# Performance work log

Measured on AMD Instinct MI355X. Metric: run time of the kernel, lower is better.

## Reference

```python
import jax, jax.numpy as jnp
import numpy as np

CHAN = 128
IN_CHAN = 3
NB_OUT = 10
K = 2  # maxPoolKer


def affine_grid(theta, H, W):
    # theta: [C,2,3] -> grid [C,H,W,2], torch F.affine_grid align_corners=False
    xs = (2.0 * jnp.arange(W, dtype=jnp.float32) + 1.0) / W - 1.0
    ys = (2.0 * jnp.arange(H, dtype=jnp.float32) + 1.0) / H - 1.0
    gx, gy = jnp.meshgrid(xs, ys)  # [H,W]
    base = jnp.stack([gx, gy, jnp.ones_like(gx)], axis=-1)  # [H,W,3]
    return jnp.einsum('crk,hwk->chwr', theta, base)  # [...,0]=x, [...,1]=y


def grid_sample(img, grid):
    # img [M,H,W], grid [M,H,W,2]; bilinear, zeros padding, align_corners=False
    M, H, W = img.shape
    ix = ((grid[..., 0] + 1.0) * W - 1.0) * 0.5
    iy = ((grid[..., 1] + 1.0) * H - 1.0) * 0.5
    x0 = jnp.floor(ix)
    y0 = jnp.floor(iy)
    wx = ix - x0
    wy = iy - y0

    def tap(xi, yi):
        valid = (xi >= 0) & (xi <= W - 1) & (yi >= 0) & (yi <= H - 1)
        xc = jnp.clip(xi, 0, W - 1).astype(jnp.int32)
        yc = jnp.clip(yi, 0, H - 1).astype(jnp.int32)
        v = jax.vmap(lambda im, y, x: im[y, x])(img, yc, xc)
        return jnp.where(valid, v, 0.0)

    v00 = tap(x0, y0)
    v01 = tap(x0 + 1.0, y0)
    v10 = tap(x0, y0 + 1.0)
    v11 = tap(x0 + 1.0, y0 + 1.0)
    return (1.0 - wy) * ((1.0 - wx) * v00 + wx * v01) + wy * ((1.0 - wx) * v10 + wx * v11)


def geom_layer(x, geo, lin, box):
    # x [B,Ci,H,W]; lin [C,Ci]; geo,box [C,2,3]
    B, Ci, H, W = x.shape
    C = lin.shape[0]
    y = jnp.einsum('ci,bihw->bchw', lin, x)  # channel linear combine
    grid = affine_grid(geo, H, W)            # [C,H,W,2], shared across batch
    samp = jax.vmap(lambda yb: grid_sample(yb, grid))(y)  # [B,C,H,W]
    bgrid = affine_grid(box, H, W)
    boxm = grid_sample(jnp.ones((C, H, W), samp.dtype), bgrid)  # BoxPool mask
    return samp * boxm[None]


def maxpool_g(x, k):
    # MaxPool2d_G: depthwise box-filter conv -> argmax -> gather window from padded x
    B, C, H, W = x.shape
    ch, cw = H // k, W // k
    ker = jnp.ones((1, 1, ch, cw), x.dtype) / (ch + cw)
    xr = x.reshape(B * C, 1, H, W)
    conv = jax.lax.conv_general_dilated(
        xr, ker, (1, 1), [(ch // 2, ch // 2), (cw // 2, cw // 2)])
    conv = conv[:, :, :H, :W].reshape(B, C, H * W)
    argm = jnp.argmax(conv, axis=-1)
    r = argm // H  # original code uses origImgSize[0]; assumes square H==W
    c = argm % W
    padH, padW = H + H // k, W + W // k
    top = padH // 2 - H // 2
    left = padW // 2 - W // 2
    padded = jnp.zeros((B, C, padH, padW), x.dtype).at[:, :, top:top + H, left:left + W].set(x)
    r2 = r + H // (2 * k)
    c2 = c + W // (2 * k)
    ri = r2[..., None] + (jnp.arange(ch) - ch // 2)  # [B,C,ch]
    ci = c2[..., None] + (jnp.arange(cw) - cw // 2)  # [B,C,cw]
    gat = jax.vmap(jax.vmap(lambda p, rr, cc: p[rr[:, None], cc[None, :]]))(padded, ri, ci)
    return gat  # [B,C,ch,cw]


def setup_inputs() -> dict:
    key = jax.random.key(0)
    ks = jax.random.split(key, 12)
    eye = jnp.eye(3, dtype=jnp.float32)[:2]  # [2,3]
    x = jax.random.normal(ks[0], (8, IN_CHAN, 64, 64), dtype=jnp.float32)
    geo0 = eye[None] + 0.1 * jax.random.normal(ks[1], (CHAN, 2, 3), dtype=jnp.float32)
    lin0 = jax.random.uniform(ks[2], (CHAN, IN_CHAN), dtype=jnp.float32)
    box0 = eye[None] + 0.1 * jax.random.normal(ks[3], (CHAN, 2, 3), dtype=jnp.float32)
    geos = eye[None, None] + 0.1 * jax.random.normal(ks[4], (3, CHAN, 2, 3), dtype=jnp.float32)
    lins = jax.random.uniform(ks[5], (3, CHAN, CHAN), dtype=jnp.float32)
    boxes = eye[None, None] + 0.1 * jax.random.normal(ks[6], (3, CHAN, 2, 3), dtype=jnp.float32)
    bound = 1.0 / np.sqrt(CHAN)
    dense_w = jax.random.uniform(ks[7], (NB_OUT, CHAN), dtype=jnp.float32, minval=-bound, maxval=bound)
    dense_b = jax.random.uniform(ks[8], (NB_OUT,), dtype=jnp.float32, minval=-bound, maxval=bound)
    return {"x": x, "geo0": geo0, "lin0": lin0, "box0": box0,
            "geos": geos, "lins": lins, "boxes": boxes,
            "dense_w": dense_w, "dense_b": dense_b}


def reference(x, geo0, lin0, box0, geos, lins, boxes, dense_w, dense_b):
    h = geom_layer(x, geo0, lin0, box0)            # inLay: [8,128,64,64]
    h = geom_layer(h, geos[0], lins[0], boxes[0])  # layer 0
    h = maxpool_g(h, K)                            # layer 1 (maxPoolPos=1): [8,128,32,32]
    h = geom_layer(h, geos[1], lins[1], boxes[1])  # layer 2
    h = geom_layer(h, geos[2], lins[2], boxes[2])  # layer 3
    feat = h
    pooled = feat.mean(axis=-1).mean(axis=-1)      # [B,C]
    out = pooled @ dense_w.T + dense_b             # [B,nbOut]
    return out, feat
```

## Files before the change

### kernel.cpp

```cpp
#include <hip/hip_runtime.h>

#define BB 8
#define CC 128

__device__ __forceinline__ float sample_pad(const float* __restrict__ pl, int stride,
                                            float WF, float ix, float iy) {
  ix = fminf(fmaxf(ix, -1.0f), WF);
  iy = fminf(fmaxf(iy, -1.0f), WF);
  float x0f = floorf(ix), y0f = floorf(iy);
  float wx = ix - x0f, wy = iy - y0f;
  int xi = (int)x0f + 1, yi = (int)y0f + 1;
  const float* p0 = pl + yi * stride + xi;
  float v00 = p0[0], v01 = p0[1], v10 = p0[stride], v11 = p0[stride + 1];
  return (1.0f - wy) * ((1.0f - wx) * v00 + wx * v01) +
         wy * ((1.0f - wx) * v10 + wx * v11);
}

__device__ __forceinline__ float box_mask(float bix, float biy, float WM1) {
  float bx0 = floorf(bix), by0 = floorf(biy);
  float bwx = bix - bx0, bwy = biy - by0;
  float mx = (((bx0 >= 0.0f) && (bx0 <= WM1)) ? (1.0f - bwx) : 0.0f) +
             (((bx0 >= -1.0f) && (bx0 <= WM1 - 1.0f)) ? bwx : 0.0f);
  float my = (((by0 >= 0.0f) && (by0 <= WM1)) ? (1.0f - bwy) : 0.0f) +
             (((by0 >= -1.0f) && (by0 <= WM1 - 1.0f)) ? bwy : 0.0f);
  return mx * my;
}

__global__ __launch_bounds__(256) void inlay_sample_kernel(
    const float* __restrict__ x, const float* __restrict__ lin,
    const float* __restrict__ geo, const float* __restrict__ box,
    const float* __restrict__ db, float* __restrict__ out,
    float* __restrict__ head) {
  const int H = 64, W = 64, HW = 4096;
  __shared__ float cp[67 * 68];
  int bc = blockIdx.x;
  int c = bc & (CC - 1);
  int b = bc >> 7;
  int tid = threadIdx.x;
  if (bc == 0 && tid < 80) head[tid] = db[tid % 10];
  const float* xb = x + (size_t)b * 3 * HW;

  float w0 = lin[c * 3 + 0], w1 = lin[c * 3 + 1], w2 = lin[c * 3 + 2];

  if (tid < 68) {
    cp[tid] = 0.0f; cp[65 * 68 + tid] = 0.0f; cp[66 * 68 + tid] = 0.0f;
  } else if (tid < 132) {
    int r = tid - 67;
    cp[r * 68 + 0] = 0.0f; cp[r * 68 + 65] = 0.0f; cp[r * 68 + 66] = 0.0f;
  }

#pragma unroll
  for (int k = 0; k < 4; ++k) {
    int i4 = tid + k * 256;
    int base = i4 * 4;
    float4 f0 = *reinterpret_cast<const float4*>(&xb[base]);
    float4 f1 = *reinterpret_cast<const float4*>(&xb[HW + base]);
    float4 f2 = *reinterpret_cast<const float4*>(&xb[2 * HW + base]);
    int h = i4 >> 4, w = (i4 & 15) * 4;
    float* d = &cp[(h + 1) * 68 + w + 1];
    d[0] = w0 * f0.x + w1 * f1.x + w2 * f2.x;
    d[1] = w0 * f0.y + w1 * f1.y + w2 * f2.y;
    d[2] = w0 * f0.z + w1 * f1.z + w2 * f2.z;
    d[3] = w0 * f0.w + w1 * f1.w + w2 * f2.w;
  }
  __syncthreads();

  const float* g = geo + c * 6;
  const float* bx = box + c * 6;
  float g0 = g[0], g1 = g[1], g2 = g[2], g3 = g[3], g4 = g[4], g5 = g[5];
  float b0 = bx[0], b1 = bx[1], b2 = bx[2], b3 = bx[3], b4 = bx[4], b5 = bx[5];
  float* o = out + ((size_t)b * CC + c) * HW;

#pragma unroll
  for (int k = 0; k < 16; ++k) {
    int px = tid + k * 256;
    int h = px >> 6, w = px & 63;
    float xs = (2.0f * w + 1.0f) / W - 1.0f;
    float ys = (2.0f * h + 1.0f) / H - 1.0f;
    float ix = ((g0 * xs + g1 * ys + g2 + 1.0f) * W - 1.0f) * 0.5f;
    float iy = ((g3 * xs + g4 * ys + g5 + 1.0f) * H - 1.0f) * 0.5f;
    float samp = sample_pad(cp, 68, 64.0f, ix, iy);
    float bix = ((b0 * xs + b1 * ys + b2 + 1.0f) * W - 1.0f) * 0.5f;
    float biy = ((b3 * xs + b4 * ys + b5 + 1.0f) * H - 1.0f) * 0.5f;
    o[px] = samp * box_mask(bix, biy, 63.0f);
  }
}

__global__ __launch_bounds__(256) void gemm64_kernel(
    const float* __restrict__ lin, const float* __restrict__ x,
    float* __restrict__ y, int HW) {
  const int Ci = 128;
  __shared__ __align__(16) float As[16][68];
  __shared__ __align__(16) float Bs[16][64];
  int b = blockIdx.z;
  const float* xb = x + (size_t)b * Ci * HW;
  float* yb = y + (size_t)b * CC * HW;
  int tid = threadIdx.x;
  int tx = tid & 15, ty = tid >> 4;
  int row0 = blockIdx.y * 64;
  int col0 = blockIdx.x * 64;
  int m = tid >> 2, kq = (tid & 3) * 4;
  int kk = tid >> 4, n4 = (tid & 15) * 4;
  float acc[4][4] = {};
  float4 ra = *reinterpret_cast<const float4*>(&lin[(row0 + m) * Ci + kq]);
  float4 rb = *reinterpret_cast<const float4*>(&xb[(size_t)kk * HW + col0 + n4]);
  for (int k0 = 0; k0 < 128; k0 += 16) {
    __syncthreads();
    As[kq + 0][m] = ra.x; As[kq + 1][m] = ra.y; As[kq + 2][m] = ra.z; As[kq + 3][m] = ra.w;
    *reinterpret_cast<float4*>(&Bs[kk][n4]) = rb;
    __syncthreads();
    if (k0 + 16 < 128) {
      ra = *reinterpret_cast<const float4*>(&lin[(row0 + m) * Ci + k0 + 16 + kq]);
      rb = *reinterpret_cast<const float4*>(&xb[(size_t)(k0 + 16 + kk) * HW + col0 + n4]);
    }
#pragma unroll
    for (int kki = 0; kki < 16; ++kki) {
      float4 a4 = *reinterpret_cast<const float4*>(&As[kki][ty * 4]);
      float4 b4 = *reinterpret_cast<const float4*>(&Bs[kki][tx * 4]);
      float a[4] = {a4.x, a4.y, a4.z, a4.w};
      float bv[4] = {b4.x, b4.y, b4.z, b4.w};
#pragma unroll
      for (int i = 0; i < 4; i++)
#pragma unroll
        for (int j = 0; j < 4; j++) acc[i][j] += a[i] * bv[j];
    }
  }
#pragma unroll
  for (int i = 0; i < 4; i++) {
    float* yr = yb + (size_t)(row0 + ty * 4 + i) * HW + col0 + tx * 4;
    *reinterpret_cast<float4*>(yr) = make_float4(acc[i][0], acc[i][1], acc[i][2], acc[i][3]);
  }
}

__global__ __launch_bounds__(256) void sampmax_kernel(
    const float* __restrict__ y, const float* __restrict__ geo,
    const float* __restrict__ box, float* __restrict__ out) {
  __shared__ __align__(16) float sp[64 * 68];
  __shared__ __align__(16) float arena[67 * 68];
  __shared__ float wv[4];
  __shared__ int wi[4];
  __shared__ int am_s;
  float* pl = arena;
  float* cb = arena;

  int bc = blockIdx.x;
  int c = bc & (CC - 1);
  int tid = threadIdx.x;

  if (tid < 68) {
    pl[tid] = 0.0f; pl[65 * 68 + tid] = 0.0f; pl[66 * 68 + tid] = 0.0f;
  } else if (tid < 132) {
    int r = tid - 67;
    pl[r * 68 + 0] = 0.0f; pl[r * 68 + 65] = 0.0f; pl[r * 68 + 66] = 0.0f;
  }
  {
    const float* plane = y + (size_t)bc * 4096;
#pragma unroll
    for (int k = 0; k < 4; ++k) {
      int i4 = tid + k * 256;
      float4 f = *reinterpret_cast<const float4*>(&plane[i4 * 4]);
      int h = i4 >> 4, w = (i4 & 15) * 4;
      float* d = &pl[(h + 1) * 68 + w + 1];
      d[0] = f.x; d[1] = f.y; d[2] = f.z; d[3] = f.w;
    }
  }
  __syncthreads();

  {
    const float* g = geo + c * 6;
    const float* bx = box + c * 6;
    float g0 = g[0], g1 = g[1], g2 = g[2], g3 = g[3], g4 = g[4], g5 = g[5];
    float b0 = bx[0], b1 = bx[1], b2 = bx[2], b3 = bx[3], b4 = bx[4], b5 = bx[5];
#pragma unroll
    for (int k = 0; k < 16; ++k) {
      int px = tid + k * 256;
      int h = px >> 6, w = px & 63;
      float xs = (2.0f * w + 1.0f) / 64.0f - 1.0f;
      float ys = (2.0f * h + 1.0f) / 64.0f - 1.0f;
      float ix = ((g0 * xs + g1 * ys + g2 + 1.0f) * 64.0f - 1.0f) * 0.5f;
      float iy = ((g3 * xs + g4 * ys + g5 + 1.0f) * 64.0f - 1.0f) * 0.5f;
      float samp = sample_pad(pl, 68, 64.0f, ix, iy);
      float bix = ((b0 * xs + b1 * ys + b2 + 1.0f) * 64.0f - 1.0f) * 0.5f;
      float biy = ((b3 * xs + b4 * ys + b5 + 1.0f) * 64.0f - 1.0f) * 0.5f;
      sp[h * 68 + w] = samp * box_mask(bix, biy, 63.0f);
    }
  }
  __syncthreads();

  {
    int strip = tid >> 4, w4 = (tid & 15) * 4;
    int h0 = strip * 4;
    float4 a = make_float4(0.f, 0.f, 0.f, 0.f);
    float4 keep0 = a, keep1 = a, keep2 = a;
#pragma unroll
    for (int j = 0; j < 32; ++j) {
      int r = h0 + j - 16;
      bool valid = (r >= 0) && (r < 64);
      int rc = valid ? r : 0;
      float4 f = *reinterpret_cast<const float4*>(&sp[rc * 68 + w4]);
      f.x = valid ? f.x : 0.0f; f.y = valid ? f.y : 0.0f;
      f.z = valid ? f.z : 0.0f; f.w = valid ? f.w : 0.0f;
      if (j == 0) keep0 = f;
      if (j == 1) keep1 = f;
      if (j == 2) keep2 = f;
      a.x += f.x; a.y += f.y; a.z += f.z; a.w += f.w;
    }
    *reinterpret_cast<float4*>(&cb[(h0 + 0) * 68 + w4]) = a;
#pragma unroll
    for (int j = 32; j < 35; ++j) {
      int r = h0 + j - 16;
      bool valid = (r < 64);
      int rc = valid ? r : 0;
      float4 f = *reinterpret_cast<const float4*>(&sp[rc * 68 + w4]);
      f.x = valid ? f.x : 0.0f; f.y = valid ? f.y : 0.0f;
      f.z = valid ? f.z : 0.0f; f.w = valid ? f.w : 0.0f;
      float4 kp = (j == 32) ? keep0 : ((j == 33) ? keep1 : keep2);
      a.x += f.x - kp.x; a.y += f.y - kp.y; a.z += f.z - kp.z; a.w += f.w - kp.w;
      *reinterpret_cast<float4*>(&cb[(h0 + j - 31) * 68 + w4]) = a;
    }
  }
  __syncthreads();

  float best = -3.402823466e+38f;
  int bidx = 0x7fffffff;
#pragma unroll
  for (int hh = 0; hh < 4; ++hh) {
    int h = (tid >> 4) + hh * 16;
    int w4 = (tid & 15) * 4;
    float s0 = 0.f, k0 = 0.f, k1 = 0.f, k2 = 0.f;
#pragma unroll
    for (int q = 0; q < 8; ++q) {
      int u0 = w4 - 16 + 4 * q;
      bool ok = (u0 >= 0) && (u0 <= 60);
      int uc = ok ? u0 : 0;
      float4 f = *reinterpret_cast<const float4*>(&cb[h * 68 + uc]);
      f.x = ok ? f.x : 0.0f; f.y = ok ? f.y : 0.0f;
      f.z = ok ? f.z : 0.0f; f.w = ok ? f.w : 0.0f;
      if (q == 0) { k0 = f.x; k1 = f.y; k2 = f.z; }
      s0 += f.x; s0 += f.y; s0 += f.z; s0 += f.w;
    }
    float ftx = 0.f, fty = 0.f, ftz = 0.f;
    {
      int u0 = w4 + 16;
      bool ok = (u0 <= 60);
      int uc = ok ? u0 : 0;
      float4 f = *reinterpret_cast<const float4*>(&cb[h * 68 + uc]);
      ftx = ok ? f.x : 0.0f; fty = ok ? f.y : 0.0f; ftz = ok ? f.z : 0.0f;
    }
    float s1 = s0 - k0 + ftx;
    float s2 = s1 - k1 + fty;
    float s3 = s2 - k2 + ftz;
    float sv[4] = {s0, s1, s2, s3};
#pragma unroll
    for (int d = 0; d < 4; ++d) {
      int i = (h << 6) + w4 + d;
      if (sv[d] > best) { best = sv[d]; bidx = i; }
    }
  }
#pragma unroll
  for (int off = 32; off > 0; off >>= 1) {
    float v2 = __shfl_down(best, off);
    int i2 = __shfl_down(bidx, off);
    if (v2 > best || (v2 == best && i2 < bidx)) { best = v2; bidx = i2; }
  }
  if ((tid & 63) == 0) { wv[tid >> 6] = best; wi[tid >> 6] = bidx; }
  __syncthreads();
  if (tid == 0) {
    float bv = wv[0]; int bi = wi[0];
#pragma unroll
    for (int k = 1; k < 4; ++k)
      if (wv[k] > bv || (wv[k] == bv && wi[k] < bi)) { bv = wv[k]; bi = wi[k]; }
    am_s = bi;
  }
  __syncthreads();

  int am = am_s;
  int r = am >> 6, cx = am & 63;
  float* o = out + (size_t)bc * 1024;
#pragma unroll
  for (int k = 0; k < 4; ++k) {
    int idx = tid + k * 256;
    int oi = idx >> 5, oj = idx & 31;
    int rr = r + oi - 16, cj = cx + oj - 16;
    bool v = (rr >= 0) && (rr < 64) && (cj >= 0) && (cj < 64);
    int rrc = v ? rr : 0, cjc = v ? cj : 0;
    o[idx] = v ? sp[rrc * 68 + cjc] : 0.0f;
  }
}

__global__ __launch_bounds__(256) void gemm32_kernel(
    const float* __restrict__ lin, const float* __restrict__ x,
    float* __restrict__ y) {
  const int Ci = 128, HW = 1024;
  __shared__ __align__(16) float As[16][36];
  __shared__ __align__(16) float Bs[16][64];
  int b = blockIdx.z;
  const float* xb = x + (size_t)b * Ci * HW;
  float* yb = y + (size_t)b * CC * HW;
  int tid = threadIdx.x;
  int tx = tid & 15, ty = tid >> 4;
  int row0 = blockIdx.y * 32;
  int col0 = blockIdx.x * 64;
  int m = tid >> 2, kq = (tid & 3) * 4;
  int kk = tid >> 4, n4 = (tid & 15) * 4;
  float acc[2][4] = {};
  float4 ra = make_float4(0.f, 0.f, 0.f, 0.f);
  if (tid < 128) ra = *reinterpret_cast<const float4*>(&lin[(row0 + m) * Ci + kq]);
  float4 rb = *reinterpret_cast<const float4*>(&xb[(size_t)kk * HW + col0 + n4]);
  for (int k0 = 0; k0 < 128; k0 += 16) {
    __syncthreads();
    if (tid < 128) { As[kq + 0][m] = ra.x; As[kq + 1][m] = ra.y; As[kq + 2][m] = ra.z; As[kq + 3][m] = ra.w; }
    *reinterpret_cast<float4*>(&Bs[kk][n4]) = rb;
    __syncthreads();
    if (k0 + 16 < 128) {
      if (tid < 128) ra = *reinterpret_cast<const float4*>(&lin[(row0 + m) * Ci + k0 + 16 + kq]);
      rb = *reinterpret_cast<const float4*>(&xb[(size_t)(k0 + 16 + kk) * HW + col0 + n4]);
    }
#pragma unroll
    for (int kki = 0; kki < 16; ++kki) {
      float a0 = As[kki][ty * 2], a1 = As[kki][ty * 2 + 1];
      float4 b4 = *reinterpret_cast<const float4*>(&Bs[kki][tx * 4]);
      acc[0][0] += a0 * b4.x; acc[0][1] += a0 * b4.y; acc[0][2] += a0 * b4.z; acc[0][3] += a0 * b4.w;
      acc[1][0] += a1 * b4.x; acc[1][1] += a1 * b4.y; acc[1][2] += a1 * b4.z; acc[1][3] += a1 * b4.w;
    }
  }
#pragma unroll
  for (int i = 0; i < 2; i++) {
    float* yr = yb + (size_t)(row0 + ty * 2 + i) * HW + col0 + tx * 4;
    *reinterpret_cast<float4*>(yr) = make_float4(acc[i][0], acc[i][1], acc[i][2], acc[i][3]);
  }
}

template <bool POOL>
__global__ __launch_bounds__(256) void sample32_kernel(
    const float* __restrict__ y, const float* __restrict__ geo,
    const float* __restrict__ box, float* __restrict__ out,
    const float* __restrict__ dw, float* __restrict__ head) {
  const int W = 32, HW = 1024;
  __shared__ float pl[35 * 36];
  __shared__ float wred[4];
  int bc = blockIdx.x;
  int c = bc & (CC - 1);
  int b = bc >> 7;
  int tid = threadIdx.x;

  if (tid < 36) {
    pl[tid] = 0.0f; pl[33 * 36 + tid] = 0.0f; pl[34 * 36 + tid] = 0.0f;
  } else if (tid < 68) {
    int r = tid - 35;
    pl[r * 36 + 0] = 0.0f; pl[r * 36 + 33] = 0.0f; pl[r * 36 + 34] = 0.0f; pl[r * 36 + 35] = 0.0f;
  }
  {
    const float* plane = y + (size_t)bc * HW;
    float4 f = *reinterpret_cast<const float4*>(&plane[tid * 4]);
    int h = tid >> 3, w = (tid & 7) * 4;
    float* d = &pl[(h + 1) * 36 + w + 1];
    d[0] = f.x; d[1] = f.y; d[2] = f.z; d[3] = f.w;
  }
  __syncthreads();

  const float* g = geo + c * 6;
  const float* bxp = box + c * 6;
  float g0 = g[0], g1 = g[1], g2 = g[2], g3 = g[3], g4 = g[4], g5 = g[5];
  float b0 = bxp[0], b1 = bxp[1], b2 = bxp[2], b3 = bxp[3], b4 = bxp[4], b5 = bxp[5];
  float* o = out + (size_t)bc * HW;
  float psum = 0.f;
#pragma unroll
  for (int k = 0; k < 4; ++k) {
    int px = tid + k * 256;
    int h = px >> 5, w = px & 31;
    float xs = (2.0f * w + 1.0f) / W - 1.0f;
    float ys = (2.0f * h + 1.0f) / W - 1.0f;
    float ix = ((g0 * xs + g1 * ys + g2 + 1.0f) * W - 1.0f) * 0.5f;
    float iy = ((g3 * xs + g4 * ys + g5 + 1.0f) * W - 1.0f) * 0.5f;
    float samp = sample_pad(pl, 36, 32.0f, ix, iy);
    float bix = ((b0 * xs + b1 * ys + b2 + 1.0f) * W - 1.0f) * 0.5f;
    float biy = ((b3 * xs + b4 * ys + b5 + 1.0f) * W - 1.0f) * 0.5f;
    float res = samp * box_mask(bix, biy, 31.0f);
    o[px] = res;
    if (POOL) psum += res;
  }
  if (POOL) {
    int lane = tid & 63, wid = tid >> 6;
    float r = psum;
#pragma unroll
    for (int off = 32; off > 0; off >>= 1) r += __shfl_down(r, off);
    if (lane == 0) wred[wid] = r;
    __syncthreads();
    if (tid < 10) {
      float t = (wred[0] + wred[1] + wred[2] + wred[3]) * (1.0f / 1024.0f);
      atomicAdd(&head[b * 10 + tid], t * dw[tid * 128 + c]);
    }
  }
}

extern "C" void kernel_launch(void* const* d_in, const int* in_sizes, int n_in,
                              void* d_out, int out_size, void* d_ws, size_t ws_size,
                              hipStream_t stream) {
  const float* x     = (const float*)d_in[0];
  const float* geo0  = (const float*)d_in[1];
  const float* lin0  = (const float*)d_in[2];
  const float* box0  = (const float*)d_in[3];
  const float* geos  = (const float*)d_in[4];
  const float* lins  = (const float*)d_in[5];
  const float* boxes = (const float*)d_in[6];
  const float* dw    = (const float*)d_in[7];
  const float* db    = (const float*)d_in[8];

  float* out  = (float*)d_out;
  float* feat = out + 80;
  float* ws   = (float*)d_ws;
  float* ws0  = ws;
  float* ws1  = ws + 4194304;
  float* ws2  = ws + 8388608;

  inlay_sample_kernel<<<dim3(BB * CC), 256, 0, stream>>>(x, lin0, geo0, box0, db, ws1, out);
  gemm64_kernel<<<dim3(64, 2, BB), 256, 0, stream>>>(lins, ws1, ws0, 4096);
  sampmax_kernel<<<dim3(BB * CC), 256, 0, stream>>>(ws0, geos, boxes, ws1);
  gemm32_kernel<<<dim3(16, 4, BB), 256, 0, stream>>>(lins + 16384, ws1, ws2);
  sample32_kernel<false><<<dim3(BB * CC), 256, 0, stream>>>(ws2, geos + 768, boxes + 768, ws0, nullptr, nullptr);
  gemm32_kernel<<<dim3(16, 4, BB), 256, 0, stream>>>(lins + 32768, ws0, ws2);
  sample32_kernel<true><<<dim3(BB * CC), 256, 0, stream>>>(ws2, geos + 1536, boxes + 1536, feat, dw, out);
}
```

Baseline: 151.7 us.

## Fuse all stages into one cooperative persistent kernel with grid syncs

Replaces the seven separate kernel launches with a single cooperative persistent kernel that loops over work units per stage and uses grid-wide syncs between stages. A shared-memory arena is reused across stages, and the original launches remain as a fallback path. The gemm32 stage is also retiled to 32x32 tiles without register prefetch, so it runs 1024 blocks. The aim is to remove launch gaps and tail effects. In exchange it adds grid barrier cost, a larger shared-memory footprint that may cap occupancy, and drops __restrict__ qualifiers.

```diff
diff --git a/kernel.cpp b/kernel.cpp
--- a/kernel.cpp
+++ b/kernel.cpp
@@ -1,9 +1,12 @@
 #include <hip/hip_runtime.h>
-
-#define BB 8
+#include <hip/hip_cooperative_groups.h>
+
+namespace cg = cooperative_groups;
+
 #define CC 128
-
-__device__ __forceinline__ float sample_pad(const float* __restrict__ pl, int stride,
+#define NUNITS 1024
+
+__device__ __forceinline__ float sample_pad(const float* pl, int stride,
                                             float WF, float ix, float iy) {
   ix = fminf(fmaxf(ix, -1.0f), WF);
   iy = fminf(fmaxf(iy, -1.0f), WF);
@@ -26,29 +29,21 @@
   return mx * my;
 }
 
-__global__ __launch_bounds__(256) void inlay_sample_kernel(
-    const float* __restrict__ x, const float* __restrict__ lin,
-    const float* __restrict__ geo, const float* __restrict__ box,
-    const float* __restrict__ db, float* __restrict__ out,
-    float* __restrict__ head) {
-  const int H = 64, W = 64, HW = 4096;
-  __shared__ float cp[67 * 68];
-  int bc = blockIdx.x;
-  int c = bc & (CC - 1);
-  int b = bc >> 7;
-  int tid = threadIdx.x;
-  if (bc == 0 && tid < 80) head[tid] = db[tid % 10];
+
+__device__ void stage_inlay(int u, int tid, float* cp, const float* x,
+                            const float* lin0, const float* geo0, const float* box0,
+                            const float* db, float* ws1, float* head) {
+  const int W = 64, HW = 4096;
+  int b = u >> 7, c = u & (CC - 1);
+  if (u == 0 && tid < 80) head[tid] = db[tid % 10];
   const float* xb = x + (size_t)b * 3 * HW;
-
-  float w0 = lin[c * 3 + 0], w1 = lin[c * 3 + 1], w2 = lin[c * 3 + 2];
-
+  float w0 = lin0[c * 3 + 0], w1 = lin0[c * 3 + 1], w2 = lin0[c * 3 + 2];
   if (tid < 68) {
     cp[tid] = 0.0f; cp[65 * 68 + tid] = 0.0f; cp[66 * 68 + tid] = 0.0f;
   } else if (tid < 132) {
     int r = tid - 67;
     cp[r * 68 + 0] = 0.0f; cp[r * 68 + 65] = 0.0f; cp[r * 68 + 66] = 0.0f;
   }
-
 #pragma unroll
   for (int k = 0; k < 4; ++k) {
     int i4 = tid + k * 256;
@@ -64,59 +59,54 @@
     d[3] = w0 * f0.w + w1 * f1.w + w2 * f2.w;
   }
   __syncthreads();
-
-  const float* g = geo + c * 6;
-  const float* bx = box + c * 6;
+  const float* g = geo0 + c * 6;
+  const float* bp = box0 + c * 6;
   float g0 = g[0], g1 = g[1], g2 = g[2], g3 = g[3], g4 = g[4], g5 = g[5];
-  float b0 = bx[0], b1 = bx[1], b2 = bx[2], b3 = bx[3], b4 = bx[4], b5 = bx[5];
-  float* o = out + ((size_t)b * CC + c) * HW;
-
+  float b0 = bp[0], b1 = bp[1], b2 = bp[2], b3 = bp[3], b4 = bp[4], b5 = bp[5];
+  float* o = ws1 + (size_t)u * HW;
 #pragma unroll
   for (int k = 0; k < 16; ++k) {
     int px = tid + k * 256;
     int h = px >> 6, w = px & 63;
     float xs = (2.0f * w + 1.0f) / W - 1.0f;
-    float ys = (2.0f * h + 1.0f) / H - 1.0f;
+    float ys = (2.0f * h + 1.0f) / W - 1.0f;
     float ix = ((g0 * xs + g1 * ys + g2 + 1.0f) * W - 1.0f) * 0.5f;
-    float iy = ((g3 * xs + g4 * ys + g5 + 1.0f) * H - 1.0f) * 0.5f;
+    float iy = ((g3 * xs + g4 * ys + g5 + 1.0f) * W - 1.0f) * 0.5f;
     float samp = sample_pad(cp, 68, 64.0f, ix, iy);
     float bix = ((b0 * xs + b1 * ys + b2 + 1.0f) * W - 1.0f) * 0.5f;
-    float biy = ((b3 * xs + b4 * ys + b5 + 1.0f) * H - 1.0f) * 0.5f;
+    float biy = ((b3 * xs + b4 * ys + b5 + 1.0f) * W - 1.0f) * 0.5f;
     o[px] = samp * box_mask(bix, biy, 63.0f);
   }
 }
 
-__global__ __launch_bounds__(256) void gemm64_kernel(
-    const float* __restrict__ lin, const float* __restrict__ x,
-    float* __restrict__ y, int HW) {
-  const int Ci = 128;
-  __shared__ __align__(16) float As[16][68];
-  __shared__ __align__(16) float Bs[16][64];
-  int b = blockIdx.z;
-  const float* xb = x + (size_t)b * Ci * HW;
-  float* yb = y + (size_t)b * CC * HW;
-  int tid = threadIdx.x;
+__device__ void stage_gemm64(int u, int tid, float* As, float* Bs,
+                             const float* lw, const float* xin, float* yout) {
+  const int Ci = 128, HW = 4096;
+  int b = u >> 7, t = u & 127;
+  int row0 = (t & 1) * 64;
+  int col0 = (t >> 1) * 64;
+  const float* xb = xin + (size_t)b * Ci * HW;
+  float* yb = yout + (size_t)b * CC * HW;
   int tx = tid & 15, ty = tid >> 4;
-  int row0 = blockIdx.y * 64;
-  int col0 = blockIdx.x * 64;
   int m = tid >> 2, kq = (tid & 3) * 4;
   int kk = tid >> 4, n4 = (tid & 15) * 4;
   float acc[4][4] = {};
-  float4 ra = *reinterpret_cast<const float4*>(&lin[(row0 + m) * Ci + kq]);
+  float4 ra = *reinterpret_cast<const float4*>(&lw[(row0 + m) * Ci + kq]);
   float4 rb = *reinterpret_cast<const float4*>(&xb[(size_t)kk * HW + col0 + n4]);
   for (int k0 = 0; k0 < 128; k0 += 16) {
     __syncthreads();
-    As[kq + 0][m] = ra.x; As[kq + 1][m] = ra.y; As[kq + 2][m] = ra.z; As[kq + 3][m] = ra.w;
-    *reinterpret_cast<float4*>(&Bs[kk][n4]) = rb;
+    As[(kq + 0) * 68 + m] = ra.x; As[(kq + 1) * 68 + m] = ra.y;
+    As[(kq + 2) * 68 + m] = ra.z; As[(kq + 3) * 68 + m] = ra.w;
+    *reinterpret_cast<float4*>(&Bs[kk * 64 + n4]) = rb;
     __syncthreads();
     if (k0 + 16 < 128) {
-      ra = *reinterpret_cast<const float4*>(&lin[(row0 + m) * Ci + k0 + 16 + kq]);
+      ra = *reinterpret_cast<const float4*>(&lw[(row0 + m) * Ci + k0 + 16 + kq]);
       rb = *reinterpret_cast<const float4*>(&xb[(size_t)(k0 + 16 + kk) * HW + col0 + n4]);
     }
 #pragma unroll
     for (int kki = 0; kki < 16; ++kki) {
-      float4 a4 = *reinterpret_cast<const float4*>(&As[kki][ty * 4]);
-      float4 b4 = *reinterpret_cast<const float4*>(&Bs[kki][tx * 4]);
+      float4 a4 = *reinterpret_cast<const float4*>(&As[kki * 68 + ty * 4]);
+      float4 b4 = *reinterpret_cast<const float4*>(&Bs[kki * 64 + tx * 4]);
       float a[4] = {a4.x, a4.y, a4.z, a4.w};
       float bv[4] = {b4.x, b4.y, b4.z, b4.w};
 #pragma unroll
@@ -132,21 +122,12 @@
   }
 }
 
-__global__ __launch_bounds__(256) void sampmax_kernel(
-    const float* __restrict__ y, const float* __restrict__ geo,
-    const float* __restrict__ box, float* __restrict__ out) {
-  __shared__ __align__(16) float sp[64 * 68];
-  __shared__ __align__(16) float arena[67 * 68];
-  __shared__ float wv[4];
-  __shared__ int wi[4];
-  __shared__ int am_s;
-  float* pl = arena;
-  float* cb = arena;
-
-  int bc = blockIdx.x;
-  int c = bc & (CC - 1);
-  int tid = threadIdx.x;
-
+__device__ void stage_sampmax(int u, int tid, float* sp, float* pl,
+                              float* wv, int* wi, int* am_s,
+                              const float* yin, const float* geo, const float* box,
+                              float* outp) {
+  float* cb = pl;
+  int c = u & (CC - 1);
   if (tid < 68) {
     pl[tid] = 0.0f; pl[65 * 68 + tid] = 0.0f; pl[66 * 68 + tid] = 0.0f;
   } else if (tid < 132) {
@@ -154,7 +135,7 @@
     pl[r * 68 + 0] = 0.0f; pl[r * 68 + 65] = 0.0f; pl[r * 68 + 66] = 0.0f;
   }
   {
-    const float* plane = y + (size_t)bc * 4096;
+    const float* plane = yin + (size_t)u * 4096;
 #pragma unroll
     for (int k = 0; k < 4; ++k) {
       int i4 = tid + k * 256;
@@ -165,12 +146,11 @@
     }
   }
   __syncthreads();
-
   {
     const float* g = geo + c * 6;
-    const float* bx = box + c * 6;
+    const float* bp = box + c * 6;
     float g0 = g[0], g1 = g[1], g2 = g[2], g3 = g[3], g4 = g[4], g5 = g[5];
-    float b0 = bx[0], b1 = bx[1], b2 = bx[2], b3 = bx[3], b4 = bx[4], b5 = bx[5];
+    float b0 = bp[0], b1 = bp[1], b2 = bp[2], b3 = bp[3], b4 = bp[4], b5 = bp[5];
 #pragma unroll
     for (int k = 0; k < 16; ++k) {
       int px = tid + k * 256;
@@ -186,7 +166,6 @@
     }
   }
   __syncthreads();
-
   {
     int strip = tid >> 4, w4 = (tid & 15) * 4;
     int h0 = strip * 4;
@@ -220,7 +199,6 @@
     }
   }
   __syncthreads();
-
   float best = -3.402823466e+38f;
   int bidx = 0x7fffffff;
 #pragma unroll
@@ -270,13 +248,12 @@
 #pragma unroll
     for (int k = 1; k < 4; ++k)
       if (wv[k] > bv || (wv[k] == bv && wi[k] < bi)) { bv = wv[k]; bi = wi[k]; }
-    am_s = bi;
-  }
-  __syncthreads();
-
-  int am = am_s;
+    *am_s = bi;
+  }
+  __syncthreads();
+  int am = *am_s;
   int r = am >> 6, cx = am & 63;
-  float* o = out + (size_t)bc * 1024;
+  float* o = outp + (size_t)u * 1024;
 #pragma unroll
   for (int k = 0; k < 4; ++k) {
     int idx = tid + k * 256;
@@ -288,62 +265,47 @@
   }
 }
 
-__global__ __launch_bounds__(256) void gemm32_kernel(
-    const float* __restrict__ lin, const float* __restrict__ x,
-    float* __restrict__ y) {
-  const int Ci = 128, HW = 1024;
-  __shared__ __align__(16) float As[16][36];
-  __shared__ __align__(16) float Bs[16][64];
-  int b = blockIdx.z;
-  const float* xb = x + (size_t)b * Ci * HW;
-  float* yb = y + (size_t)b * CC * HW;
-  int tid = threadIdx.x;
-  int tx = tid & 15, ty = tid >> 4;
-  int row0 = blockIdx.y * 32;
-  int col0 = blockIdx.x * 64;
-  int m = tid >> 2, kq = (tid & 3) * 4;
-  int kk = tid >> 4, n4 = (tid & 15) * 4;
-  float acc[2][4] = {};
-  float4 ra = make_float4(0.f, 0.f, 0.f, 0.f);
-  if (tid < 128) ra = *reinterpret_cast<const float4*>(&lin[(row0 + m) * Ci + kq]);
-  float4 rb = *reinterpret_cast<const float4*>(&xb[(size_t)kk * HW + col0 + n4]);
+__device__ void stage_gemm32(int u, int tid, float* As, float* Bs,
+                             const float* lw, const float* xin, float* yout) {
+  int b = u >> 7, t = u & 127;
+  int row0 = (t >> 5) * 32, col0 = (t & 31) * 32;
+  const float* xb = xin + (size_t)b * 128 * 1024;
+  float* yb = yout + (size_t)b * 128 * 1024;
+  int ty = tid >> 4, tx = tid & 15;
+  int am_ = tid >> 2, akq = (tid & 3) * 4;
+  int bl = tid - 128, bkk = bl >> 3, bn4 = (bl & 7) * 4;
+  float acc00 = 0.f, acc01 = 0.f, acc10 = 0.f, acc11 = 0.f;
   for (int k0 = 0; k0 < 128; k0 += 16) {
     __syncthreads();
-    if (tid < 128) { As[kq + 0][m] = ra.x; As[kq + 1][m] = ra.y; As[kq + 2][m] = ra.z; As[kq + 3][m] = ra.w; }
-    *reinterpret_cast<float4*>(&Bs[kk][n4]) = rb;
-    __syncthreads();
-    if (k0 + 16 < 128) {
-      if (tid < 128) ra = *reinterpret_cast<const float4*>(&lin[(row0 + m) * Ci + k0 + 16 + kq]);
-      rb = *reinterpret_cast<const float4*>(&xb[(size_t)(k0 + 16 + kk) * HW + col0 + n4]);
-    }
+    if (tid < 128) {
+      float4 ra = *reinterpret_cast<const float4*>(&lw[(row0 + am_) * 128 + k0 + akq]);
+      As[(akq + 0) * 36 + am_] = ra.x; As[(akq + 1) * 36 + am_] = ra.y;
+      As[(akq + 2) * 36 + am_] = ra.z; As[(akq + 3) * 36 + am_] = ra.w;
+    } else {
+      float4 rb = *reinterpret_cast<const float4*>(&xb[(size_t)(k0 + bkk) * 1024 + col0 + bn4]);
+      *reinterpret_cast<float4*>(&Bs[bkk * 32 + bn4]) = rb;
+    }
+    __syncthreads();
 #pragma unroll
     for (int kki = 0; kki < 16; ++kki) {
-      float a0 = As[kki][ty * 2], a1 = As[kki][ty * 2 + 1];
-      float4 b4 = *reinterpret_cast<const float4*>(&Bs[kki][tx * 4]);
-      acc[0][0] += a0 * b4.x; acc[0][1] += a0 * b4.y; acc[0][2] += a0 * b4.z; acc[0][3] += a0 * b4.w;
-      acc[1][0] += a1 * b4.x; acc[1][1] += a1 * b4.y; acc[1][2] += a1 * b4.z; acc[1][3] += a1 * b4.w;
-    }
-  }
-#pragma unroll
-  for (int i = 0; i < 2; i++) {
-    float* yr = yb + (size_t)(row0 + ty * 2 + i) * HW + col0 + tx * 4;
-    *reinterpret_cast<float4*>(yr) = make_float4(acc[i][0], acc[i][1], acc[i][2], acc[i][3]);
-  }
+      float2 av = *reinterpret_cast<const float2*>(&As[kki * 36 + ty * 2]);
+      float2 bv = *reinterpret_cast<const float2*>(&Bs[kki * 32 + tx * 2]);
+      acc00 += av.x * bv.x; acc01 += av.x * bv.y;
+      acc10 += av.y * bv.x; acc11 += av.y * bv.y;
+    }
+  }
+  *reinterpret_cast<float2*>(&yb[(size_t)(row0 + ty * 2) * 1024 + col0 + tx * 2]) =
+      make_float2(acc00, acc01);
+  *reinterpret_cast<float2*>(&yb[(size_t)(row0 + ty * 2 + 1) * 1024 + col0 + tx * 2]) =
+      make_float2(acc10, acc11);
 }
 
 template <bool POOL>
-__global__ __launch_bounds__(256) void sample32_kernel(
-    const float* __restrict__ y, const float* __restrict__ geo,
-    const float* __restrict__ box, float* __restrict__ out,
-    const float* __restrict__ dw, float* __restrict__ head) {
-  const int W = 32, HW = 1024;
-  __shared__ float pl[35 * 36];
-  __shared__ float wred[4];
-  int bc = blockIdx.x;
-  int c = bc & (CC - 1);
-  int b = bc >> 7;
-  int tid = threadIdx.x;
-
+__device__ void stage_sample32(int u, int tid, float* pl, float* wred,
+                               const float* yin, const float* geo, const float* box,
+                               float* outp, const float* dw, float* head) {
+  const int W = 32;
+  int b = u >> 7, c = u & (CC - 1);
   if (tid < 36) {
     pl[tid] = 0.0f; pl[33 * 36 + tid] = 0.0f; pl[34 * 36 + tid] = 0.0f;
   } else if (tid < 68) {
@@ -351,19 +313,18 @@
     pl[r * 36 + 0] = 0.0f; pl[r * 36 + 33] = 0.0f; pl[r * 36 + 34] = 0.0f; pl[r * 36 + 35] = 0.0f;
   }
   {
-    const float* plane = y + (size_t)bc * HW;
+    const float* plane = yin + (size_t)u * 1024;
     float4 f = *reinterpret_cast<const float4*>(&plane[tid * 4]);
     int h = tid >> 3, w = (tid & 7) * 4;
     float* d = &pl[(h + 1) * 36 + w + 1];
     d[0] = f.x; d[1] = f.y; d[2] = f.z; d[3] = f.w;
   }
   __syncthreads();
-
   const float* g = geo + c * 6;
-  const float* bxp = box + c * 6;
+  const float* bp = box + c * 6;
   float g0 = g[0], g1 = g[1], g2 = g[2], g3 = g[3], g4 = g[4], g5 = g[5];
-  float b0 = bxp[0], b1 = bxp[1], b2 = bxp[2], b3 = bxp[3], b4 = bxp[4], b5 = bxp[5];
-  float* o = out + (size_t)bc * HW;
+  float b0 = bp[0], b1 = bp[1], b2 = bp[2], b3 = bp[3], b4 = bp[4], b5 = bp[5];
+  float* o = outp + (size_t)u * 1024;
   float psum = 0.f;
 #pragma unroll
   for (int k = 0; k < 4; ++k) {
@@ -382,16 +343,106 @@
   }
   if (POOL) {
     int lane = tid & 63, wid = tid >> 6;
-    float r = psum;
-#pragma unroll
-    for (int off = 32; off > 0; off >>= 1) r += __shfl_down(r, off);
-    if (lane == 0) wred[wid] = r;
+#pragma unroll
+    for (int off = 32; off > 0; off >>= 1) psum += __shfl_down(psum, off);
+    if (lane == 0) wred[wid] = psum;
     __syncthreads();
     if (tid < 10) {
-      float t = (wred[0] + wred[1] + wred[2] + wred[3]) * (1.0f / 1024.0f);
-      atomicAdd(&head[b * 10 + tid], t * dw[tid * 128 + c]);
-    }
-  }
+      float tsum = (wred[0] + wred[1] + wred[2] + wred[3]) * (1.0f / 1024.0f);
+      atomicAdd(&head[b * 10 + tid], tsum * dw[tid * 128 + c]);
+    }
+  }
+}
+
+__global__ __launch_bounds__(256, 4) void meganet_kernel(
+    const float* x, const float* geo0, const float* lin0, const float* box0,
+    const float* geos, const float* lins, const float* boxes, const float* dw,
+    const float* db, float* out, float* ws0, float* ws1, float* ws2) {
+  cg::grid_group grid = cg::this_grid();
+  __shared__ __align__(16) float arena[8908];
+  __shared__ float wv[4];
+  __shared__ int wi[4];
+  __shared__ int am_s;
+  float* feat = out + 80;
+  int tid = threadIdx.x;
+  const int NB = gridDim.x;
+
+  for (int u = blockIdx.x; u < NUNITS; u += NB) {
+    __syncthreads();
+    stage_inlay(u, tid, arena, x, lin0, geo0, box0, db, ws1, out);
+  }
+  grid.sync();
+  for (int u = blockIdx.x; u < NUNITS; u += NB) {
+    __syncthreads();
+    stage_gemm64(u, tid, arena, arena + 1088, lins, ws1, ws0);
+  }
+  grid.sync();
+  for (int u = blockIdx.x; u < NUNITS; u += NB) {
+    __syncthreads();
+    stage_sampmax(u, tid, arena, arena + 4352, wv, wi, &am_s, ws0, geos, boxes, ws1);
+  }
+  grid.sync();
+  for (int u = blockIdx.x; u < NUNITS; u += NB) {
+    __syncthreads();
+    stage_gemm32(u, tid, arena, arena + 576, lins + 16384, ws1, ws2);
+  }
+  grid.sync();
+  for (int u = blockIdx.x; u < NUNITS; u += NB) {
+    __syncthreads();
+    stage_sample32<false>(u, tid, arena, wv, ws2, geos + 768, boxes + 768, ws0,
+                          nullptr, nullptr);
+  }
+  grid.sync();
+  for (int u = blockIdx.x; u < NUNITS; u += NB) {
+    __syncthreads();
+    stage_gemm32(u, tid, arena, arena + 576, lins + 32768, ws0, ws2);
+  }
+  grid.sync();
+  for (int u = blockIdx.x; u < NUNITS; u += NB) {
+    __syncthreads();
+    stage_sample32<true>(u, tid, arena, wv, ws2, geos + 1536, boxes + 1536, feat,
+                         dw, out);
+  }
+}
+
+__global__ __launch_bounds__(256) void k_inlay(
+    const float* x, const float* lin0, const float* geo0, const float* box0,
+    const float* db, float* ws1, float* head) {
+  __shared__ __align__(16) float cp[67 * 68];
+  stage_inlay(blockIdx.x, threadIdx.x, cp, x, lin0, geo0, box0, db, ws1, head);
+}
+
+__global__ __launch_bounds__(256) void k_gemm64(
+    const float* lw, const float* xin, float* yout) {
+  __shared__ __align__(16) float As[16 * 68];
+  __shared__ __align__(16) float Bs[16 * 64];
+  stage_gemm64(blockIdx.x, threadIdx.x, As, Bs, lw, xin, yout);
+}
+
+__global__ __launch_bounds__(256) void k_sampmax(
+    const float* yin, const float* geo, const float* box, float* outp) {
+  __shared__ __align__(16) float sp[64 * 68];
+  __shared__ __align__(16) float pl[67 * 68];
+  __shared__ float wv[4];
+  __shared__ int wi[4];
+  __shared__ int am_s;
+  stage_sampmax(blockIdx.x, threadIdx.x, sp, pl, wv, wi, &am_s, yin, geo, box, outp);
+}
+
+__global__ __launch_bounds__(256) void k_gemm32(
+    const float* lw, const float* xin, float* yout) {
+  __shared__ __align__(16) float As[16 * 36];
+  __shared__ __align__(16) float Bs[16 * 32];
+  stage_gemm32(blockIdx.x, threadIdx.x, As, Bs, lw, xin, yout);
+}
+
+template <bool POOL>
+__global__ __launch_bounds__(256) void k_sample32(
+    const float* yin, const float* geo, const float* box, float* outp,
+    const float* dw, float* head) {
+  __shared__ float pl[35 * 36];
+  __shared__ float wred[4];
+  stage_sample32<POOL>(blockIdx.x, threadIdx.x, pl, wred, yin, geo, box, outp, dw, head);
 }
 
 extern "C" void kernel_launch(void* const* d_in, const int* in_sizes, int n_in,
@@ -414,11 +465,44 @@
   float* ws1  = ws + 4194304;
   float* ws2  = ws + 8388608;
 
-  inlay_sample_kernel<<<dim3(BB * CC), 256, 0, stream>>>(x, lin0, geo0, box0, db, ws1, out);
-  gemm64_kernel<<<dim3(64, 2, BB), 256, 0, stream>>>(lins, ws1, ws0, 4096);
-  sampmax_kernel<<<dim3(BB * CC), 256, 0, stream>>>(ws0, geos, boxes, ws1);
-  gemm32_kernel<<<dim3(16, 4, BB), 256, 0, stream>>>(lins + 16384, ws1, ws2);
-  sample32_kernel<false><<<dim3(BB * CC), 256, 0, stream>>>(ws2, geos + 768, boxes + 768, ws0, nullptr, nullptr);
-  gemm32_kernel<<<dim3(16, 4, BB), 256, 0, stream>>>(lins + 32768, ws0, ws2);
-  sample32_kernel<true><<<dim3(BB * CC), 256, 0, stream>>>(ws2, geos + 1536, boxes + 1536, feat, dw, out);
-}
+  static int coop_grid = -2;
+  if (coop_grid == -2) {
+    int occ = 0, cus = 0, dev = 0;
+    if (hipGetDevice(&dev) == hipSuccess &&
+        hipDeviceGetAttribute(&cus, hipDeviceAttributeMultiprocessorCount, dev) == hipSuccess &&
+        hipOccupancyMaxActiveBlocksPerMultiprocessor(
+            &occ, (const void*)meganet_kernel, 256, 0) == hipSuccess &&
+        occ > 0 && cus > 0) {
+      long cap = (long)occ * (long)cus;
+      coop_grid = (int)(cap < NUNITS ? cap : NUNITS);
+      if (coop_grid < 8) coop_grid = -1;
+    } else {
+      coop_grid = -1;
+    }
+  }
+
+  bool done = false;
+  if (coop_grid > 0) {
+    void* args[] = {(void*)&x, (void*)&geo0, (void*)&lin0, (void*)&box0,
+                    (void*)&geos, (void*)&lins, (void*)&boxes, (void*)&dw,
+                    (void*)&db, (void*)&out, (void*)&ws0, (void*)&ws1, (void*)&ws2};
+    hipError_t e = hipLaunchCooperativeKernel(
+        reinterpret_cast<void*>(meganet_kernel), dim3(coop_grid), dim3(256),
+        args, 0, stream);
+    if (e == hipSuccess) {
+      done = true;
+    } else {
+      coop_grid = -1;
+    }
+  }
+
+  if (!done) {
+    k_inlay<<<dim3(NUNITS), 256, 0, stream>>>(x, lin0, geo0, box0, db, ws1, out);
+    k_gemm64<<<dim3(NUNITS), 256, 0, stream>>>(lins, ws1, ws0);
+    k_sampmax<<<dim3(NUNITS), 256, 0, stream>>>(ws0, geos, boxes, ws1);
+    k_gemm32<<<dim3(NUNITS), 256, 0, stream>>>(lins + 16384, ws1, ws2);
+    k_sample32<false><<<dim3(NUNITS), 256, 0, stream>>>(ws2, geos + 768, boxes + 768, ws0, nullptr, nullptr);
+    k_gemm32<<<dim3(NUNITS), 256, 0, stream>>>(lins + 32768, ws0, ws2);
+    k_sample32<true><<<dim3(NUNITS), 256, 0, stream>>>(ws2, geos + 1536, boxes + 1536, feat, dw, out);
+  }
+}
```

New measurement: 417.9 us. 2.75x slower.

## Use fp16 MFMA for the 64x64 channel-mixing GEMM

Applied to the files above, without the earlier changes.

Replaces the scalar FP32 register-tiled GEMM for the layer-0 channel combine with a kernel that converts A and B tiles to fp16, stages the full K=128 in LDS, and computes with 16x16x16 f16 MFMA instructions. The aim is to offload the FMA work to matrix cores and drop the per-k-step sync loop. The output stores become scalar and strided per lane rather than float4, and the fp16 inputs reduce precision, which risks accuracy against the fp32 reference.

```diff
diff --git a/kernel.cpp b/kernel.cpp
--- a/kernel.cpp
+++ b/kernel.cpp
@@ -2,6 +2,9 @@
 
 #define BB 8
 #define CC 128
+
+typedef _Float16 f16x4 __attribute__((ext_vector_type(4)));
+typedef float f32x4 __attribute__((ext_vector_type(4)));
 
 __device__ __forceinline__ float sample_pad(const float* __restrict__ pl, int stride,
                                             float WF, float ix, float iy) {
@@ -86,49 +89,76 @@
   }
 }
 
-__global__ __launch_bounds__(256) void gemm64_kernel(
+__global__ __launch_bounds__(256) void gemm64_mfma_kernel(
     const float* __restrict__ lin, const float* __restrict__ x,
-    float* __restrict__ y, int HW) {
-  const int Ci = 128;
-  __shared__ __align__(16) float As[16][68];
-  __shared__ __align__(16) float Bs[16][64];
+    float* __restrict__ y) {
+  const int Ci = 128, HW = 4096;
+  __shared__ unsigned int A_lds[64 * 66];
+  __shared__ unsigned int B_lds[64 * 66];
   int b = blockIdx.z;
+  int row0 = blockIdx.y * 64, col0 = blockIdx.x * 64;
   const float* xb = x + (size_t)b * Ci * HW;
   float* yb = y + (size_t)b * CC * HW;
   int tid = threadIdx.x;
-  int tx = tid & 15, ty = tid >> 4;
-  int row0 = blockIdx.y * 64;
-  int col0 = blockIdx.x * 64;
-  int m = tid >> 2, kq = (tid & 3) * 4;
-  int kk = tid >> 4, n4 = (tid & 15) * 4;
-  float acc[4][4] = {};
-  float4 ra = *reinterpret_cast<const float4*>(&lin[(row0 + m) * Ci + kq]);
-  float4 rb = *reinterpret_cast<const float4*>(&xb[(size_t)kk * HW + col0 + n4]);
-  for (int k0 = 0; k0 < 128; k0 += 16) {
-    __syncthreads();
-    As[kq + 0][m] = ra.x; As[kq + 1][m] = ra.y; As[kq + 2][m] = ra.z; As[kq + 3][m] = ra.w;
-    *reinterpret_cast<float4*>(&Bs[kk][n4]) = rb;
-    __syncthreads();
-    if (k0 + 16 < 128) {
-      ra = *reinterpret_cast<const float4*>(&lin[(row0 + m) * Ci + k0 + 16 + kq]);
-      rb = *reinterpret_cast<const float4*>(&xb[(size_t)(k0 + 16 + kk) * HW + col0 + n4]);
-    }
-#pragma unroll
-    for (int kki = 0; kki < 16; ++kki) {
-      float4 a4 = *reinterpret_cast<const float4*>(&As[kki][ty * 4]);
-      float4 b4 = *reinterpret_cast<const float4*>(&Bs[kki][tx * 4]);
-      float a[4] = {a4.x, a4.y, a4.z, a4.w};
-      float bv[4] = {b4.x, b4.y, b4.z, b4.w};
-#pragma unroll
-      for (int i = 0; i < 4; i++)
-#pragma unroll
-        for (int j = 0; j < 4; j++) acc[i][j] += a[i] * bv[j];
-    }
-  }
-#pragma unroll
-  for (int i = 0; i < 4; i++) {
-    float* yr = yb + (size_t)(row0 + ty * 4 + i) * HW + col0 + tx * 4;
-    *reinterpret_cast<float4*>(yr) = make_float4(acc[i][0], acc[i][1], acc[i][2], acc[i][3]);
+
+  {
+    int row = tid >> 2, kc = (tid & 3) * 32;
+    const float* ap = &lin[(row0 + row) * Ci + kc];
+    unsigned int* dst = &A_lds[row * 66 + (kc >> 1)];
+#pragma unroll
+    for (int i = 0; i < 8; ++i) {
+      float4 v = *reinterpret_cast<const float4*>(ap + i * 4);
+      union { _Float16 h[2]; unsigned int u; } p0, p1;
+      p0.h[0] = (_Float16)v.x; p0.h[1] = (_Float16)v.y;
+      p1.h[0] = (_Float16)v.z; p1.h[1] = (_Float16)v.w;
+      dst[i * 2] = p0.u; dst[i * 2 + 1] = p1.u;
+    }
+  }
+  {
+    int kp = tid >> 2, cg = (tid & 3) * 16;
+    const float* b0p = &xb[(size_t)(2 * kp) * HW + col0 + cg];
+    const float* b1p = &xb[(size_t)(2 * kp + 1) * HW + col0 + cg];
+#pragma unroll
+    for (int q = 0; q < 4; ++q) {
+      float4 v0 = *reinterpret_cast<const float4*>(b0p + q * 4);
+      float4 v1 = *reinterpret_cast<const float4*>(b1p + q * 4);
+      float e0[4] = {v0.x, v0.y, v0.z, v0.w};
+      float e1[4] = {v1.x, v1.y, v1.z, v1.w};
+#pragma unroll
+      for (int c = 0; c < 4; ++c) {
+        union { _Float16 h[2]; unsigned int u; } p;
+        p.h[0] = (_Float16)e0[c]; p.h[1] = (_Float16)e1[c];
+        B_lds[(cg + q * 4 + c) * 66 + kp] = p.u;
+      }
+    }
+  }
+  __syncthreads();
+
+  int w = tid >> 6, l = tid & 63;
+  int lr = l & 15, lq = l >> 4;
+  f32x4 acc0 = {0.f, 0.f, 0.f, 0.f};
+  f32x4 acc1 = acc0, acc2 = acc0, acc3 = acc0;
+  const unsigned int* arow = &A_lds[(w * 16 + lr) * 66 + 2 * lq];
+  const unsigned int* bcol = &B_lds[lr * 66 + 2 * lq];
+#pragma unroll
+  for (int s = 0; s < 8; ++s) {
+    f16x4 af = *reinterpret_cast<const f16x4*>(arow + s * 8);
+    f16x4 b0 = *reinterpret_cast<const f16x4*>(bcol + 0 * 16 * 66 + s * 8);
+    f16x4 b1 = *reinterpret_cast<const f16x4*>(bcol + 1 * 16 * 66 + s * 8);
+    f16x4 b2 = *reinterpret_cast<const f16x4*>(bcol + 2 * 16 * 66 + s * 8);
+    f16x4 b3 = *reinterpret_cast<const f16x4*>(bcol + 3 * 16 * 66 + s * 8);
+    acc0 = __builtin_amdgcn_mfma_f32_16x16x16f16(af, b0, acc0, 0, 0, 0);
+    acc1 = __builtin_amdgcn_mfma_f32_16x16x16f16(af, b1, acc1, 0, 0, 0);
+    acc2 = __builtin_amdgcn_mfma_f32_16x16x16f16(af, b2, acc2, 0, 0, 0);
+    acc3 = __builtin_amdgcn_mfma_f32_16x16x16f16(af, b3, acc3, 0, 0, 0);
+  }
+#pragma unroll
+  for (int i = 0; i < 4; ++i) {
+    float* yr = yb + (size_t)(row0 + w * 16 + lq * 4 + i) * HW + col0 + lr;
+    yr[0]  = acc0[i];
+    yr[16] = acc1[i];
+    yr[32] = acc2[i];
+    yr[48] = acc3[i];
   }
 }
 
@@ -415,7 +445,7 @@
   float* ws2  = ws + 8388608;
 
   inlay_sample_kernel<<<dim3(BB * CC), 256, 0, stream>>>(x, lin0, geo0, box0, db, ws1, out);
-  gemm64_kernel<<<dim3(64, 2, BB), 256, 0, stream>>>(lins, ws1, ws0, 4096);
+  gemm64_mfma_kernel<<<dim3(64, 2, BB), 256, 0, stream>>>(lins, ws1, ws0);
   sampmax_kernel<<<dim3(BB * CC), 256, 0, stream>>>(ws0, geos, boxes, ws1);
   gemm32_kernel<<<dim3(16, 4, BB), 256, 0, stream>>>(lins + 16384, ws1, ws2);
   sample32_kernel<false><<<dim3(BB * CC), 256, 0, stream>>>(ws2, geos + 768, boxes + 768, ws0, nullptr, nullptr);
```

After: 146.6 us. 1.03x faster.
